# Performance work log

Hardware: AMD Instinct MI355X
Metric: run time of the kernel (lower is better)

The kernel has to match this reference:

```python
import jax, jax.numpy as jnp
import numpy as np

L = 8        # len_prog
E = 8        # experts per layer (uniform dsl_num)
D = 256      # embed_dim
B = 16384    # batch_size
H1, H2 = 64, 32  # MyMLP hidden dims


def setup_inputs() -> dict:
    key = jax.random.key(0)
    ks = jax.random.split(key, 8)
    s1 = 1.0 / np.sqrt(D)
    s2 = 1.0 / np.sqrt(H1)
    s3 = 1.0 / np.sqrt(H2)
    return {
        "src_embeddings": jax.random.normal(ks[0], (B, D), jnp.float32),
        "W1": jax.random.normal(ks[1], (L, E, H1, D), jnp.float32) * s1,
        "b1": jax.random.normal(ks[2], (L, E, H1), jnp.float32) * s1,
        "W2": jax.random.normal(ks[3], (L, E, H2, H1), jnp.float32) * s2,
        "b2": jax.random.normal(ks[4], (L, E, H2), jnp.float32) * s2,
        "W3": jax.random.normal(ks[5], (L, E, D, H2), jnp.float32) * s3,
        "b3": jax.random.normal(ks[6], (L, E, D), jnp.float32) * s3,
        "masks": jax.random.normal(ks[7], (L, B, E), jnp.float32) * 0.1,
    }


def reference(src_embeddings, W1, b1, W2, b2, W3, b3, masks):
    # Per layer: run E small expert MLPs on the same x, then combine with
    # softmax(mask) over the expert axis (torch path: masks=None -> softmax).
    def layer(x, params):
        w1, bb1, w2, bb2, w3, bb3, m = params
        h = jax.nn.relu(jnp.einsum('bd,ehd->beh', x, w1) + bb1)      # [B,E,H1]
        h = jax.nn.relu(jnp.einsum('beh,ekh->bek', h, w2) + bb2)     # [B,E,H2]
        out = jnp.einsum('bek,edk->bed', h, w3) + bb3                # [B,E,D]
        w = jax.nn.softmax(m, axis=-1)                               # [B,E]
        x_new = jnp.einsum('be,bed->bd', w, out)                     # [B,D]
        return x_new, None

    x, _ = jax.lax.scan(layer, src_embeddings, (W1, b1, W2, b2, W3, b3, masks))
    return x
```

## Files before the change

kernel.cpp:

```cpp
#include <hip/hip_runtime.h>
#include <hip/hip_bf16.h>

#define LNUM 8
#define ENUM 8
#define DDIM 256
#define BSZ  16384
#define H1N  64
#define H2N  32

#define BT   32
#define NTHR 256

#define PX   264
#define PH1  72
#define PH2  40
#define PSW  9

#define WS1_OFF 0
#define WS2_OFF 1048576
#define WS3_OFF 1179648

typedef float f32x4 __attribute__((ext_vector_type(4)));
typedef unsigned short u16x8 __attribute__((ext_vector_type(8)));
typedef unsigned short u16x4 __attribute__((ext_vector_type(4)));
typedef __bf16 bf16x8 __attribute__((ext_vector_type(8)));

#define Z4 ((f32x4){0.f, 0.f, 0.f, 0.f})

static __device__ __forceinline__ unsigned short f2bf(float f) {
    __bf16 h = (__bf16)f;
    return __builtin_bit_cast(unsigned short, h);
}

static __device__ __forceinline__ f32x4 mfma16(u16x8 a, u16x8 b, f32x4 c) {
    return __builtin_amdgcn_mfma_f32_16x16x32_bf16(
        __builtin_bit_cast(bf16x8, a), __builtin_bit_cast(bf16x8, b), c, 0, 0, 0);
}

static __device__ __forceinline__ void lbar() {
    asm volatile("s_waitcnt lgkmcnt(0)" ::: "memory");
    __builtin_amdgcn_s_barrier();
    asm volatile("" ::: "memory");
}

__global__ __launch_bounds__(256) void cvt_w_frag(
    const float* __restrict__ w1, const float* __restrict__ w2,
    const float* __restrict__ w3, unsigned short* __restrict__ ws)
{
    int gid = blockIdx.x * 256 + threadIdx.x;
    const float* src;
    unsigned short* dst;
    if (gid < 131072) {
        int s = gid >> 11, rem = gid & 2047;
        int n = rem >> 5, kc = rem & 31;
        int nt = n >> 4, r = n & 15, kt = kc >> 2, q = kc & 3;
        src = w1 + (size_t)gid * 8;
        dst = ws + WS1_OFF + (size_t)s * 16384 + nt * 4096 + kt * 512 + (q * 16 + r) * 8;
    } else if (gid < 147456) {
        int g = gid - 131072;
        int s = g >> 8, rem = g & 255;
        int n = rem >> 3, kc = rem & 7;
        int n2 = n >> 4, r = n & 15, kt = kc >> 2, q = kc & 3;
        src = w2 + (size_t)g * 8;
        dst = ws + WS2_OFF + (size_t)s * 2048 + n2 * 1024 + kt * 512 + (q * 16 + r) * 8;
    } else {
        int g = gid - 147456;
        int s = g >> 10, rem = g & 1023;
        int n = rem >> 2, q = rem & 3;
        int nt = n >> 4, r = n & 15;
        src = w3 + (size_t)g * 8;
        dst = ws + WS3_OFF + (size_t)s * 8192 + nt * 512 + (q * 16 + r) * 8;
    }
    float4 a = *(const float4*)src;
    float4 b = *(const float4*)(src + 4);
    u16x8 p;
    p[0] = f2bf(a.x); p[1] = f2bf(a.y); p[2] = f2bf(a.z); p[3] = f2bf(a.w);
    p[4] = f2bf(b.x); p[5] = f2bf(b.y); p[6] = f2bf(b.z); p[7] = f2bf(b.w);
    *(u16x8*)dst = p;
}

__global__ __launch_bounds__(NTHR, 2) void moe_fused(
    const float* __restrict__ src, const unsigned short* __restrict__ Wf,
    const float* __restrict__ b1, const float* __restrict__ b2,
    const float* __restrict__ b3, const float* __restrict__ masks,
    float* __restrict__ out)
{
    __shared__ __align__(16) unsigned short Xlds[BT * PX];
    __shared__ __align__(16) unsigned short H1W[4][BT * PH1];
    __shared__ __align__(16) unsigned short H2T[8][BT * PH2];
    __shared__ float SWlds[BT * PSW];

    const int tid  = threadIdx.x;
    const int lane = tid & 63;
    const int wv   = tid >> 6;
    const int n15  = lane & 15;
    const int q    = lane >> 4;
    const int b0   = blockIdx.x * BT;

    const unsigned short* w3base = Wf + WS3_OFF + wv * 2048 + lane * 8;

    u16x8 xf[2][8];
    f32x4 ACC[2][4];

    auto stage_softmax = [&](int l) {
        if (tid < BT) {
            const float* mp = masks + ((size_t)l * BSZ + b0 + tid) * ENUM;
            float4 m0 = *(const float4*)mp;
            float4 m1 = *(const float4*)(mp + 4);
            float mv[8] = {m0.x, m0.y, m0.z, m0.w, m1.x, m1.y, m1.z, m1.w};
            float mx = mv[0];
            #pragma unroll
            for (int e = 1; e < 8; ++e) mx = fmaxf(mx, mv[e]);
            float s = 0.f;
            #pragma unroll
            for (int e = 0; e < 8; ++e) { mv[e] = expf(mv[e] - mx); s += mv[e]; }
            float inv = 1.f / s;
            #pragma unroll
            for (int e = 0; e < 8; ++e) SWlds[tid * PSW + e] = mv[e] * inv;
        }
    };

    auto acc_init = [&](int l) {
        const float* b3l = b3 + (size_t)l * ENUM * DDIM;
        #pragma unroll
        for (int mt = 0; mt < 2; ++mt)
            #pragma unroll
            for (int nt = 0; nt < 4; ++nt) ACC[mt][nt] = Z4;
        #pragma unroll 2
        for (int e2 = 0; e2 < ENUM; ++e2) {
            float swv[2][4];
            #pragma unroll
            for (int mt = 0; mt < 2; ++mt)
                #pragma unroll
                for (int rr = 0; rr < 4; ++rr)
                    swv[mt][rr] = SWlds[(mt*16 + q*4 + rr) * PSW + e2];
            #pragma unroll
            for (int nt = 0; nt < 4; ++nt) {
                float bv = b3l[e2 * DDIM + wv*64 + nt*16 + n15];
                #pragma unroll
                for (int mt = 0; mt < 2; ++mt)
                    #pragma unroll
                    for (int rr = 0; rr < 4; ++rr)
                        ACC[mt][nt][rr] += swv[mt][rr] * bv;
            }
        }
    };

    auto xf_read = [&]() {
        #pragma unroll
        for (int mt = 0; mt < 2; ++mt)
            #pragma unroll
            for (int kt = 0; kt < 8; ++kt)
                xf[mt][kt] = *(const u16x8*)
                    &Xlds[(mt*16 + n15) * PX + q*8 + kt*32];
    };
    auto x_write = [&]() {
        #pragma unroll
        for (int mt = 0; mt < 2; ++mt)
            #pragma unroll
            for (int nt = 0; nt < 4; ++nt)
                #pragma unroll
                for (int rr = 0; rr < 4; ++rr)
                    Xlds[(mt*16 + q*4 + rr) * PX + wv*64 + nt*16 + n15] =
                        f2bf(ACC[mt][nt][rr]);
    };

    #pragma unroll
    for (int i = 0; i < 4; ++i) {
        int o = (i * NTHR + tid) * 8;
        int r = o >> 8, c = o & 255;
        const float* p = src + (size_t)(b0 + r) * DDIM + c;
        float4 f0 = *(const float4*)(p);
        float4 f1 = *(const float4*)(p + 4);
        u16x8 pk;
        pk[0] = f2bf(f0.x); pk[1] = f2bf(f0.y); pk[2] = f2bf(f0.z); pk[3] = f2bf(f0.w);
        pk[4] = f2bf(f1.x); pk[5] = f2bf(f1.y); pk[6] = f2bf(f1.z); pk[7] = f2bf(f1.w);
        *(u16x8*)&Xlds[r * PX + c] = pk;
    }
    stage_softmax(0);
    __syncthreads();
    xf_read();

    #pragma unroll 1
    for (int l = 0; l < LNUM; ++l) {
        const int sbase = l * ENUM;

        #pragma unroll
        for (int pe = 0; pe < 2; ++pe) {
            const int e = wv + pe * 4;
            const int s = sbase + e;

            #pragma unroll
            for (int ft = 0; ft < 4; ++ft) {
                u16x8 w1f[8];
                const unsigned short* p1 =
                    Wf + WS1_OFF + (size_t)s * 16384 + ft * 4096 + lane * 8;
                #pragma unroll
                for (int kt = 0; kt < 8; ++kt)
                    w1f[kt] = *(const u16x8*)(p1 + kt * 512);
                f32x4 a1[2] = {Z4, Z4};
                #pragma unroll
                for (int kt = 0; kt < 8; ++kt) {
                    a1[0] = mfma16(w1f[kt], xf[0][kt], a1[0]);
                    a1[1] = mfma16(w1f[kt], xf[1][kt], a1[1]);
                }
                const float4 bb1 = *(const float4*)(b1 + s * 64 + ft * 16 + q * 4);
                #pragma unroll
                for (int mt = 0; mt < 2; ++mt) {
                    u16x4 pk;
                    #pragma unroll
                    for (int rr = 0; rr < 4; ++rr)
                        pk[rr] = f2bf(fmaxf(a1[mt][rr] + bb1[rr], 0.f));
                    *(u16x4*)&H1W[wv][(mt*16 + n15) * PH1 + ft*16 + q*4] = pk;
                }
            }

            {
                u16x8 w2f[2][2];
                const unsigned short* p2 =
                    Wf + WS2_OFF + (size_t)s * 2048 + lane * 8;
                #pragma unroll
                for (int f2 = 0; f2 < 2; ++f2)
                    #pragma unroll
                    for (int kt = 0; kt < 2; ++kt)
                        w2f[f2][kt] = *(const u16x8*)(p2 + f2*1024 + kt*512);
                u16x8 h1f[2][2];
                #pragma unroll
                for (int mt = 0; mt < 2; ++mt)
                    #pragma unroll
                    for (int kt = 0; kt < 2; ++kt)
                        h1f[mt][kt] = *(const u16x8*)
                            &H1W[wv][(mt*16 + n15) * PH1 + q*8 + kt*32];
                f32x4 a2[2][2] = {{Z4, Z4}, {Z4, Z4}};
                #pragma unroll
                for (int f2 = 0; f2 < 2; ++f2)
                    #pragma unroll
                    for (int mt = 0; mt < 2; ++mt)
                        #pragma unroll
                        for (int kt = 0; kt < 2; ++kt)
                            a2[f2][mt] = mfma16(w2f[f2][kt], h1f[mt][kt], a2[f2][mt]);
                float swv[2];
                #pragma unroll
                for (int mt = 0; mt < 2; ++mt)
                    swv[mt] = SWlds[(mt*16 + n15) * PSW + e];
                #pragma unroll
                for (int f2 = 0; f2 < 2; ++f2) {
                    const float4 bb2 = *(const float4*)(b2 + s * 32 + f2 * 16 + q * 4);
                    #pragma unroll
                    for (int mt = 0; mt < 2; ++mt) {
                        u16x4 pk;
                        #pragma unroll
                        for (int rr = 0; rr < 4; ++rr)
                            pk[rr] = f2bf(fmaxf(a2[f2][mt][rr] + bb2[rr], 0.f) * swv[mt]);
                        *(u16x4*)&H2T[e][(mt*16 + n15) * PH2 + f2*16 + q*4] = pk;
                    }
                }
            }
        }

        lbar();

        acc_init(l);

        #pragma unroll
        for (int e = 0; e < ENUM; ++e) {
            const int s = sbase + e;
            u16x8 w3f[4];
            const unsigned short* p3 = w3base + (size_t)s * 8192;
            #pragma unroll
            for (int nt = 0; nt < 4; ++nt)
                w3f[nt] = *(const u16x8*)(p3 + nt * 512);
            u16x8 h0 = *(const u16x8*)&H2T[e][(n15) * PH2 + q*8];
            u16x8 h1v = *(const u16x8*)&H2T[e][(16 + n15) * PH2 + q*8];
            #pragma unroll
            for (int nt = 0; nt < 4; ++nt) {
                ACC[0][nt] = mfma16(h0,  w3f[nt], ACC[0][nt]);
                ACC[1][nt] = mfma16(h1v, w3f[nt], ACC[1][nt]);
            }
        }

        if (l < LNUM - 1) {
            x_write();
            lbar();
            xf_read();
            stage_softmax(l + 1);
            lbar();
        }
    }

    #pragma unroll
    for (int mt = 0; mt < 2; ++mt)
        #pragma unroll
        for (int nt = 0; nt < 4; ++nt)
            #pragma unroll
            for (int rr = 0; rr < 4; ++rr)
                out[(size_t)(b0 + mt*16 + q*4 + rr) * DDIM
                    + wv*64 + nt*16 + n15] = ACC[mt][nt][rr];
}

extern "C" void kernel_launch(void* const* d_in, const int* in_sizes, int n_in,
                              void* d_out, int out_size, void* d_ws, size_t ws_size,
                              hipStream_t stream) {
    const float* src   = (const float*)d_in[0];
    const float* W1    = (const float*)d_in[1];
    const float* b1    = (const float*)d_in[2];
    const float* W2    = (const float*)d_in[3];
    const float* b2    = (const float*)d_in[4];
    const float* W3    = (const float*)d_in[5];
    const float* b3    = (const float*)d_in[6];
    const float* masks = (const float*)d_in[7];
    float* out = (float*)d_out;
    unsigned short* ws = (unsigned short*)d_ws;

    hipLaunchKernelGGL(cvt_w_frag, dim3(832), dim3(256), 0, stream, W1, W2, W3, ws);
    hipLaunchKernelGGL(moe_fused, dim3(BSZ / BT), dim3(NTHR), 0, stream,
                       src, ws, b1, b2, b3, masks, out);
}
```

Measured before the change: 175.5 us.

## Use 8 waves per block: one expert per wave, split output rows

Doubles the block to 512 threads so each of the 8 waves computes one expert's first two MLP layers instead of each of 4 waves handling two experts serially. In the final projection the waves split into two row halves by four column groups, which halves the per-wave accumulator registers. The intent is more parallelism and occupancy per block with shorter serial chains. The cost is larger LDS use (8 H1 buffers), a tighter register budget under launch bounds of 4, and more waves contending at the barriers.

```diff
diff --git a/kernel.cpp b/kernel.cpp
--- a/kernel.cpp
+++ b/kernel.cpp
@@ -9,7 +9,7 @@
 #define H2N  32
 
 #define BT   32
-#define NTHR 256
+#define NTHR 512
 
 #define PX   264
 #define PH1  72
@@ -79,28 +79,30 @@
     *(u16x8*)dst = p;
 }
 
-__global__ __launch_bounds__(NTHR, 2) void moe_fused(
+__global__ __launch_bounds__(NTHR, 4) void moe_fused(
     const float* __restrict__ src, const unsigned short* __restrict__ Wf,
     const float* __restrict__ b1, const float* __restrict__ b2,
     const float* __restrict__ b3, const float* __restrict__ masks,
     float* __restrict__ out)
 {
     __shared__ __align__(16) unsigned short Xlds[BT * PX];
-    __shared__ __align__(16) unsigned short H1W[4][BT * PH1];
+    __shared__ __align__(16) unsigned short H1W[8][BT * PH1];
     __shared__ __align__(16) unsigned short H2T[8][BT * PH2];
     __shared__ float SWlds[BT * PSW];
 
     const int tid  = threadIdx.x;
     const int lane = tid & 63;
     const int wv   = tid >> 6;
+    const int rh   = wv >> 2;
+    const int cg   = wv & 3;
     const int n15  = lane & 15;
     const int q    = lane >> 4;
     const int b0   = blockIdx.x * BT;
 
-    const unsigned short* w3base = Wf + WS3_OFF + wv * 2048 + lane * 8;
+    const unsigned short* w3base = Wf + WS3_OFF + cg * 2048 + lane * 8;
 
     u16x8 xf[2][8];
-    f32x4 ACC[2][4];
+    f32x4 ACC[4];
 
     auto stage_softmax = [&](int l) {
         if (tid < BT) {
@@ -123,25 +125,19 @@
     auto acc_init = [&](int l) {
         const float* b3l = b3 + (size_t)l * ENUM * DDIM;
         #pragma unroll
-        for (int mt = 0; mt < 2; ++mt)
-            #pragma unroll
-            for (int nt = 0; nt < 4; ++nt) ACC[mt][nt] = Z4;
+        for (int nt = 0; nt < 4; ++nt) ACC[nt] = Z4;
         #pragma unroll 2
         for (int e2 = 0; e2 < ENUM; ++e2) {
-            float swv[2][4];
-            #pragma unroll
-            for (int mt = 0; mt < 2; ++mt)
+            float swv[4];
+            #pragma unroll
+            for (int rr = 0; rr < 4; ++rr)
+                swv[rr] = SWlds[(rh*16 + q*4 + rr) * PSW + e2];
+            #pragma unroll
+            for (int nt = 0; nt < 4; ++nt) {
+                float bv = b3l[e2 * DDIM + cg*64 + nt*16 + n15];
                 #pragma unroll
                 for (int rr = 0; rr < 4; ++rr)
-                    swv[mt][rr] = SWlds[(mt*16 + q*4 + rr) * PSW + e2];
-            #pragma unroll
-            for (int nt = 0; nt < 4; ++nt) {
-                float bv = b3l[e2 * DDIM + wv*64 + nt*16 + n15];
-                #pragma unroll
-                for (int mt = 0; mt < 2; ++mt)
-                    #pragma unroll
-                    for (int rr = 0; rr < 4; ++rr)
-                        ACC[mt][nt][rr] += swv[mt][rr] * bv;
+                    ACC[nt][rr] += swv[rr] * bv;
             }
         }
     };
@@ -156,17 +152,15 @@
     };
     auto x_write = [&]() {
         #pragma unroll
-        for (int mt = 0; mt < 2; ++mt)
-            #pragma unroll
-            for (int nt = 0; nt < 4; ++nt)
-                #pragma unroll
-                for (int rr = 0; rr < 4; ++rr)
-                    Xlds[(mt*16 + q*4 + rr) * PX + wv*64 + nt*16 + n15] =
-                        f2bf(ACC[mt][nt][rr]);
+        for (int nt = 0; nt < 4; ++nt)
+            #pragma unroll
+            for (int rr = 0; rr < 4; ++rr)
+                Xlds[(rh*16 + q*4 + rr) * PX + cg*64 + nt*16 + n15] =
+                    f2bf(ACC[nt][rr]);
     };
 
     #pragma unroll
-    for (int i = 0; i < 4; ++i) {
+    for (int i = 0; i < 2; ++i) {
         int o = (i * NTHR + tid) * 8;
         int r = o >> 8, c = o & 255;
         const float* p = src + (size_t)(b0 + r) * DDIM + c;
@@ -184,78 +178,72 @@
     #pragma unroll 1
     for (int l = 0; l < LNUM; ++l) {
         const int sbase = l * ENUM;
-
-        #pragma unroll
-        for (int pe = 0; pe < 2; ++pe) {
-            const int e = wv + pe * 4;
-            const int s = sbase + e;
-
-            #pragma unroll
-            for (int ft = 0; ft < 4; ++ft) {
-                u16x8 w1f[8];
-                const unsigned short* p1 =
-                    Wf + WS1_OFF + (size_t)s * 16384 + ft * 4096 + lane * 8;
-                #pragma unroll
-                for (int kt = 0; kt < 8; ++kt)
-                    w1f[kt] = *(const u16x8*)(p1 + kt * 512);
-                f32x4 a1[2] = {Z4, Z4};
-                #pragma unroll
-                for (int kt = 0; kt < 8; ++kt) {
-                    a1[0] = mfma16(w1f[kt], xf[0][kt], a1[0]);
-                    a1[1] = mfma16(w1f[kt], xf[1][kt], a1[1]);
-                }
-                const float4 bb1 = *(const float4*)(b1 + s * 64 + ft * 16 + q * 4);
+        const int s = sbase + wv;
+
+        #pragma unroll
+        for (int ft = 0; ft < 4; ++ft) {
+            u16x8 w1f[8];
+            const unsigned short* p1 =
+                Wf + WS1_OFF + (size_t)s * 16384 + ft * 4096 + lane * 8;
+            #pragma unroll
+            for (int kt = 0; kt < 8; ++kt)
+                w1f[kt] = *(const u16x8*)(p1 + kt * 512);
+            f32x4 a1[2] = {Z4, Z4};
+            #pragma unroll
+            for (int kt = 0; kt < 8; ++kt) {
+                a1[0] = mfma16(w1f[kt], xf[0][kt], a1[0]);
+                a1[1] = mfma16(w1f[kt], xf[1][kt], a1[1]);
+            }
+            const float4 bb1 = *(const float4*)(b1 + s * 64 + ft * 16 + q * 4);
+            #pragma unroll
+            for (int mt = 0; mt < 2; ++mt) {
+                u16x4 pk;
+                #pragma unroll
+                for (int rr = 0; rr < 4; ++rr)
+                    pk[rr] = f2bf(fmaxf(a1[mt][rr] + bb1[rr], 0.f));
+                *(u16x4*)&H1W[wv][(mt*16 + n15) * PH1 + ft*16 + q*4] = pk;
+            }
+        }
+
+        {
+            u16x8 w2f[2][2];
+            const unsigned short* p2 = Wf + WS2_OFF + (size_t)s * 2048 + lane * 8;
+            #pragma unroll
+            for (int f2 = 0; f2 < 2; ++f2)
+                #pragma unroll
+                for (int kt = 0; kt < 2; ++kt)
+                    w2f[f2][kt] = *(const u16x8*)(p2 + f2*1024 + kt*512);
+            u16x8 h1f[2][2];
+            #pragma unroll
+            for (int mt = 0; mt < 2; ++mt)
+                #pragma unroll
+                for (int kt = 0; kt < 2; ++kt)
+                    h1f[mt][kt] = *(const u16x8*)
+                        &H1W[wv][(mt*16 + n15) * PH1 + q*8 + kt*32];
+            f32x4 a2[2][2] = {{Z4, Z4}, {Z4, Z4}};
+            #pragma unroll
+            for (int f2 = 0; f2 < 2; ++f2)
+                #pragma unroll
+                for (int mt = 0; mt < 2; ++mt)
+                    #pragma unroll
+                    for (int kt = 0; kt < 2; ++kt)
+                        a2[f2][mt] = mfma16(w2f[f2][kt], h1f[mt][kt], a2[f2][mt]);
+            float swv[2];
+            #pragma unroll
+            for (int mt = 0; mt < 2; ++mt)
+                swv[mt] = SWlds[(mt*16 + n15) * PSW + wv];
+            #pragma unroll
+            for (int f2 = 0; f2 < 2; ++f2) {
+                const float4 bb2 = *(const float4*)(b2 + s * 32 + f2 * 16 + q * 4);
                 #pragma unroll
                 for (int mt = 0; mt < 2; ++mt) {
                     u16x4 pk;
                     #pragma unroll
                     for (int rr = 0; rr < 4; ++rr)
-                        pk[rr] = f2bf(fmaxf(a1[mt][rr] + bb1[rr], 0.f));
-                    *(u16x4*)&H1W[wv][(mt*16 + n15) * PH1 + ft*16 + q*4] = pk;
+                        pk[rr] = f2bf(fmaxf(a2[f2][mt][rr] + bb2[rr], 0.f) * swv[mt]);
+                    *(u16x4*)&H2T[wv][(mt*16 + n15) * PH2 + f2*16 + q*4] = pk;
                 }
             }
-
-            {
-                u16x8 w2f[2][2];
-                const unsigned short* p2 =
-                    Wf + WS2_OFF + (size_t)s * 2048 + lane * 8;
-                #pragma unroll
-                for (int f2 = 0; f2 < 2; ++f2)
-                    #pragma unroll
-                    for (int kt = 0; kt < 2; ++kt)
-                        w2f[f2][kt] = *(const u16x8*)(p2 + f2*1024 + kt*512);
-                u16x8 h1f[2][2];
-                #pragma unroll
-                for (int mt = 0; mt < 2; ++mt)
-                    #pragma unroll
-                    for (int kt = 0; kt < 2; ++kt)
-                        h1f[mt][kt] = *(const u16x8*)
-                            &H1W[wv][(mt*16 + n15) * PH1 + q*8 + kt*32];
-                f32x4 a2[2][2] = {{Z4, Z4}, {Z4, Z4}};
-                #pragma unroll
-                for (int f2 = 0; f2 < 2; ++f2)
-                    #pragma unroll
-                    for (int mt = 0; mt < 2; ++mt)
-                        #pragma unroll
-                        for (int kt = 0; kt < 2; ++kt)
-                            a2[f2][mt] = mfma16(w2f[f2][kt], h1f[mt][kt], a2[f2][mt]);
-                float swv[2];
-                #pragma unroll
-                for (int mt = 0; mt < 2; ++mt)
-                    swv[mt] = SWlds[(mt*16 + n15) * PSW + e];
-                #pragma unroll
-                for (int f2 = 0; f2 < 2; ++f2) {
-                    const float4 bb2 = *(const float4*)(b2 + s * 32 + f2 * 16 + q * 4);
-                    #pragma unroll
-                    for (int mt = 0; mt < 2; ++mt) {
-                        u16x4 pk;
-                        #pragma unroll
-                        for (int rr = 0; rr < 4; ++rr)
-                            pk[rr] = f2bf(fmaxf(a2[f2][mt][rr] + bb2[rr], 0.f) * swv[mt]);
-                        *(u16x4*)&H2T[e][(mt*16 + n15) * PH2 + f2*16 + q*4] = pk;
-                    }
-                }
-            }
         }
 
         lbar();
@@ -264,19 +252,15 @@
 
         #pragma unroll
         for (int e = 0; e < ENUM; ++e) {
-            const int s = sbase + e;
             u16x8 w3f[4];
-            const unsigned short* p3 = w3base + (size_t)s * 8192;
+            const unsigned short* p3 = w3base + (size_t)(sbase + e) * 8192;
             #pragma unroll
             for (int nt = 0; nt < 4; ++nt)
                 w3f[nt] = *(const u16x8*)(p3 + nt * 512);
-            u16x8 h0 = *(const u16x8*)&H2T[e][(n15) * PH2 + q*8];
-            u16x8 h1v = *(const u16x8*)&H2T[e][(16 + n15) * PH2 + q*8];
-            #pragma unroll
-            for (int nt = 0; nt < 4; ++nt) {
-                ACC[0][nt] = mfma16(h0,  w3f[nt], ACC[0][nt]);
-                ACC[1][nt] = mfma16(h1v, w3f[nt], ACC[1][nt]);
-            }
+            u16x8 h = *(const u16x8*)&H2T[e][(rh*16 + n15) * PH2 + q*8];
+            #pragma unroll
+            for (int nt = 0; nt < 4; ++nt)
+                ACC[nt] = mfma16(h, w3f[nt], ACC[nt]);
         }
 
         if (l < LNUM - 1) {
@@ -289,13 +273,11 @@
     }
 
     #pragma unroll
-    for (int mt = 0; mt < 2; ++mt)
-        #pragma unroll
-        for (int nt = 0; nt < 4; ++nt)
-            #pragma unroll
-            for (int rr = 0; rr < 4; ++rr)
-                out[(size_t)(b0 + mt*16 + q*4 + rr) * DDIM
-                    + wv*64 + nt*16 + n15] = ACC[mt][nt][rr];
+    for (int nt = 0; nt < 4; ++nt)
+        #pragma unroll
+        for (int rr = 0; rr < 4; ++rr)
+            out[(size_t)(b0 + rh*16 + q*4 + rr) * DDIM
+                + cg*64 + nt*16 + n15] = ACC[nt][rr];
 }
 
 extern "C" void kernel_launch(void* const* d_in, const int* in_sizes, int n_in,
```

After: 228.5 us. 30.2% more time.

## Double-buffer softmax weights to drop a barrier and split MFMA accumulator chains

Applied to the files above, without the earlier changes.

The softmax weight buffer gets two copies. The next layer's softmax is computed right after the mid-layer barrier into the alternate copy, which removes the trailing barrier at the end of each layer. The softmax work is also spread across the four waves, eight lanes each, instead of being done only by the first 32 threads of one wave. The layer-1 MFMA reduction uses two independent accumulator chains (even and odd k) to cut dependency latency, at the cost of extra registers and one extra add.

```diff
diff --git a/kernel.cpp b/kernel.cpp
--- a/kernel.cpp
+++ b/kernel.cpp
@@ -88,7 +88,7 @@
     __shared__ __align__(16) unsigned short Xlds[BT * PX];
     __shared__ __align__(16) unsigned short H1W[4][BT * PH1];
     __shared__ __align__(16) unsigned short H2T[8][BT * PH2];
-    __shared__ float SWlds[BT * PSW];
+    __shared__ float SWlds[2][BT * PSW];
 
     const int tid  = threadIdx.x;
     const int lane = tid & 63;
@@ -102,9 +102,10 @@
     u16x8 xf[2][8];
     f32x4 ACC[2][4];
 
-    auto stage_softmax = [&](int l) {
-        if (tid < BT) {
-            const float* mp = masks + ((size_t)l * BSZ + b0 + tid) * ENUM;
+    auto stage_softmax = [&](int l, int p) {
+        if (lane < 8) {
+            int row = wv * 8 + lane;
+            const float* mp = masks + ((size_t)l * BSZ + b0 + row) * ENUM;
             float4 m0 = *(const float4*)mp;
             float4 m1 = *(const float4*)(mp + 4);
             float mv[8] = {m0.x, m0.y, m0.z, m0.w, m1.x, m1.y, m1.z, m1.w};
@@ -116,12 +117,13 @@
             for (int e = 0; e < 8; ++e) { mv[e] = expf(mv[e] - mx); s += mv[e]; }
             float inv = 1.f / s;
             #pragma unroll
-            for (int e = 0; e < 8; ++e) SWlds[tid * PSW + e] = mv[e] * inv;
+            for (int e = 0; e < 8; ++e) SWlds[p][row * PSW + e] = mv[e] * inv;
         }
     };
 
     auto acc_init = [&](int l) {
         const float* b3l = b3 + (size_t)l * ENUM * DDIM;
+        const int p = l & 1;
         #pragma unroll
         for (int mt = 0; mt < 2; ++mt)
             #pragma unroll
@@ -133,7 +135,7 @@
             for (int mt = 0; mt < 2; ++mt)
                 #pragma unroll
                 for (int rr = 0; rr < 4; ++rr)
-                    swv[mt][rr] = SWlds[(mt*16 + q*4 + rr) * PSW + e2];
+                    swv[mt][rr] = SWlds[p][(mt*16 + q*4 + rr) * PSW + e2];
             #pragma unroll
             for (int nt = 0; nt < 4; ++nt) {
                 float bv = b3l[e2 * DDIM + wv*64 + nt*16 + n15];
@@ -177,7 +179,7 @@
         pk[4] = f2bf(f1.x); pk[5] = f2bf(f1.y); pk[6] = f2bf(f1.z); pk[7] = f2bf(f1.w);
         *(u16x8*)&Xlds[r * PX + c] = pk;
     }
-    stage_softmax(0);
+    stage_softmax(0, 0);
     __syncthreads();
     xf_read();
 
@@ -198,11 +200,13 @@
                 #pragma unroll
                 for (int kt = 0; kt < 8; ++kt)
                     w1f[kt] = *(const u16x8*)(p1 + kt * 512);
-                f32x4 a1[2] = {Z4, Z4};
-                #pragma unroll
-                for (int kt = 0; kt < 8; ++kt) {
-                    a1[0] = mfma16(w1f[kt], xf[0][kt], a1[0]);
-                    a1[1] = mfma16(w1f[kt], xf[1][kt], a1[1]);
+                f32x4 a1e[2] = {Z4, Z4}, a1o[2] = {Z4, Z4};
+                #pragma unroll
+                for (int kt = 0; kt < 8; kt += 2) {
+                    a1e[0] = mfma16(w1f[kt],   xf[0][kt],   a1e[0]);
+                    a1e[1] = mfma16(w1f[kt],   xf[1][kt],   a1e[1]);
+                    a1o[0] = mfma16(w1f[kt+1], xf[0][kt+1], a1o[0]);
+                    a1o[1] = mfma16(w1f[kt+1], xf[1][kt+1], a1o[1]);
                 }
                 const float4 bb1 = *(const float4*)(b1 + s * 64 + ft * 16 + q * 4);
                 #pragma unroll
@@ -210,7 +214,7 @@
                     u16x4 pk;
                     #pragma unroll
                     for (int rr = 0; rr < 4; ++rr)
-                        pk[rr] = f2bf(fmaxf(a1[mt][rr] + bb1[rr], 0.f));
+                        pk[rr] = f2bf(fmaxf(a1e[mt][rr] + a1o[mt][rr] + bb1[rr], 0.f));
                     *(u16x4*)&H1W[wv][(mt*16 + n15) * PH1 + ft*16 + q*4] = pk;
                 }
             }
@@ -242,7 +246,7 @@
                 float swv[2];
                 #pragma unroll
                 for (int mt = 0; mt < 2; ++mt)
-                    swv[mt] = SWlds[(mt*16 + n15) * PSW + e];
+                    swv[mt] = SWlds[l & 1][(mt*16 + n15) * PSW + e];
                 #pragma unroll
                 for (int f2 = 0; f2 < 2; ++f2) {
                     const float4 bb2 = *(const float4*)(b2 + s * 32 + f2 * 16 + q * 4);
@@ -260,17 +264,18 @@
 
         lbar();
 
+        if (l < LNUM - 1) stage_softmax(l + 1, (l + 1) & 1);
+
         acc_init(l);
 
         #pragma unroll
         for (int e = 0; e < ENUM; ++e) {
-            const int s = sbase + e;
             u16x8 w3f[4];
-            const unsigned short* p3 = w3base + (size_t)s * 8192;
+            const unsigned short* p3 = w3base + (size_t)(sbase + e) * 8192;
             #pragma unroll
             for (int nt = 0; nt < 4; ++nt)
                 w3f[nt] = *(const u16x8*)(p3 + nt * 512);
-            u16x8 h0 = *(const u16x8*)&H2T[e][(n15) * PH2 + q*8];
+            u16x8 h0  = *(const u16x8*)&H2T[e][(n15) * PH2 + q*8];
             u16x8 h1v = *(const u16x8*)&H2T[e][(16 + n15) * PH2 + q*8];
             #pragma unroll
             for (int nt = 0; nt < 4; ++nt) {
@@ -283,8 +288,6 @@
             x_write();
             lbar();
             xf_read();
-            stage_softmax(l + 1);
-            lbar();
         }
     }
 
```

Result: no change. 177.8 us (+1.3%).
